# Performance work log

Hardware: AMD Instinct MI355X
Metric: run time of the kernel (lower is better)

The kernel has to match this reference:

```python
import jax, jax.numpy as jnp
import numpy as np

NUM = 8          # group_heads
ALPHA = 1000.0   # Pos_Enc alpha
BETA = 100.0     # Pos_Enc beta


def setup_inputs() -> dict:
    key = jax.random.key(0)
    ks = jax.random.split(key, 19)
    N, C, H = 16384, 64, 1024
    gs1 = H // NUM
    s = 0.02
    r = lambda k, shp: jax.random.normal(k, shp, dtype=jnp.float32) * s
    return {
        "features": jax.random.normal(ks[0], (N, C), dtype=jnp.float32),
        "fc1_w": r(ks[1], (C, H)), "fc1_b": r(ks[2], (H,)),
        "fc2_w": r(ks[3], (H, C)), "fc2_b": r(ks[4], (C,)),
        "g1_w": r(ks[5], (H, H)), "g1_b": r(ks[6], (H,)),
        "g2_w": r(ks[7], (H, H)), "g2_b": r(ks[8], (H,)),
        "gg1_w": r(ks[9], (gs1, gs1)), "gg1_b": r(ks[10], (gs1,)),
        "gg2_w": r(ks[11], (gs1, gs1)), "gg2_b": r(ks[12], (gs1,)),
        "wq": r(ks[13], (H, H)), "wk": r(ks[14], (H, H)), "wv": r(ks[15], (H, H)),
        "wq2": r(ks[16], (gs1, gs1)), "wk2": r(ks[17], (gs1, gs1)),
        "lpe": jax.random.normal(ks[18], (1,), dtype=jnp.float32) * 0.1,
    }


def _mlp(x, w1, b1, w2, b2):
    return jax.nn.relu(x @ w1 + b1) @ w2 + b2


def reference(features, fc1_w, fc1_b, fc2_w, fc2_b, g1_w, g1_b, g2_w, g2_b,
              gg1_w, gg1_b, gg2_w, gg2_b, wq, wk, wv, wq2, wk2, lpe):
    N, C = features.shape
    H = fc1_w.shape[1]
    gs1 = H // NUM   # feature-group size
    gs2 = N // NUM   # token-group size

    x = features @ fc1_w + fc1_b                      # (N, H)

    # --- attn1: per-feature-group vector attention (shared weights -> vectorized)
    xg = x.reshape(N, NUM, gs1)                       # contiguous feature slices
    q1 = xg @ wq2
    k1 = xg @ wk2
    h1 = _mlp(q1 - k1, gg1_w, gg1_b, gg2_w, gg2_b)
    attn1 = jax.nn.softmax(h1 / np.sqrt(gs1).astype(np.float32), axis=0)
    attn1 = attn1.reshape(N, H)                       # concat over groups = reshape

    # --- attn2: source bug: loop uses stale i=NUM-1, so the LAST token group
    # is processed NUM times and tiled along tokens.
    gf2 = x[(NUM - 1) * gs2:, :]                      # (gs2, H)
    q2 = gf2 @ wq
    k2 = gf2 @ wk
    h2 = _mlp(q2 - k2, g1_w, g1_b, g2_w, g2_b)
    a2 = jax.nn.softmax(h2 / np.sqrt(H).astype(np.float32), axis=0)
    attn2 = jnp.tile(a2, (NUM, 1))                    # (N, H)

    attn = attn1 + attn2
    v = x @ wv                                        # (N, H)

    # --- sinusoidal positional encoding (Pos_Enc), only coord-0 slice survives
    xyz = features[:, :3]                             # (N, 3)
    feat_dim = H // 2
    feat_range = jnp.arange(feat_dim, dtype=jnp.float32)
    dim_embed = jnp.power(jnp.float32(ALPHA), feat_range / feat_dim)
    div = BETA * xyz[..., None] / dim_embed           # (N, 3, feat_dim)
    emb = jnp.concatenate([jnp.sin(div), jnp.cos(div)], axis=-1)  # (N, 3, H)
    pe = (emb + lpe[0]) * lpe[0]
    pe0 = pe[:, 0, :]                                 # (N, H) first coordinate

    res = attn * (v + pe0)                            # elementwise einsum bmf,bmf->bmf
    out = res @ fc2_w + fc2_b + features              # residual
    return out
```

## Files before the change

### kernel.cpp

```cpp
#include <hip/hip_runtime.h>
#include <hip/hip_bf16.h>
#include <math.h>
#include <type_traits>


typedef __attribute__((ext_vector_type(8))) short short8;
typedef __attribute__((ext_vector_type(4))) float f32x4;
typedef __attribute__((ext_vector_type(4))) float float4v;

#define GLOAD_LDS16(gptr, lptr)                                                 \
    __builtin_amdgcn_global_load_lds(                                           \
        (const __attribute__((address_space(1))) void*)(gptr),                  \
        (__attribute__((address_space(3))) void*)(lptr), 16, 0, 0)

static __device__ __forceinline__ unsigned short f2bf_bits(float v) {
    __hip_bfloat16 h = __float2bfloat16(v);
    return __builtin_bit_cast(unsigned short, h);
}
static __device__ __forceinline__ float bf_bits2f(unsigned short u) {
    return __bfloat162float(__builtin_bit_cast(__hip_bfloat16, u));
}
static __device__ __forceinline__ int swz16(int r, int c16) {
    return (r << 4) + (c16 ^ (r & 7));
}
static __device__ __forceinline__ int swz_elem(int r, int c) {
    return (r << 7) + ((((c << 1) ^ ((r & 7) << 4))) >> 1);
}
static __device__ __forceinline__ int xcd_swz(int bid, int nwg) {
    return (bid & 7) * (nwg >> 3) + (bid >> 3);
}

static __device__ void conv_t_dev(const float* __restrict__ A, const float* __restrict__ Bsub,
                                  __hip_bfloat16* __restrict__ Ot, int K, int N,
                                  int bx, int by, int tid, float* t )
{
    const int n0 = bx * 32, k0 = by * 32;
    const int tx = tid & 31, ty = tid >> 5;
    #pragma unroll
    for (int j = 0; j < 4; ++j) {
        int k = k0 + ty + j * 8;
        float v = A[(long)k * N + n0 + tx];
        if (Bsub) v -= Bsub[(long)k * N + n0 + tx];
        t[(ty + j * 8) * 33 + tx] = v;
    }
    __syncthreads();
    #pragma unroll
    for (int j = 0; j < 4; ++j) {
        int n = n0 + ty + j * 8;
        Ot[(long)n * K + k0 + tx] = __float2bfloat16(t[tx * 33 + ty + j * 8]);
    }
}

static __device__ void xgemm_dev(const float* __restrict__ features,
                                 const float* __restrict__ fc1_w,
                                 const float* __restrict__ fc1_b,
                                 __hip_bfloat16* __restrict__ xb,
                                 int tile, int tid, char* smem)
{
    unsigned short* As = (unsigned short*)smem;
    unsigned short* Bs = (unsigned short*)(smem + 16384);
    const int bm = (tile >> 3) << 7, bn = (tile & 7) << 7;
    const int wid = tid >> 6, lane = tid & 63;
    const int wm = (wid >> 1) << 6, wn = (wid & 1) << 6;
    const int l15 = lane & 15, kg = lane >> 4;

    #pragma unroll
    for (int i = 0; i < 8; ++i) {
        int idx = i * 256 + tid;
        int r = idx >> 4, c4 = idx & 15;
        float4v f = *(const float4v*)(features + (long)(bm + r) * 64 + c4 * 4);
        unsigned int p0 = f2bf_bits(f[0]) | ((unsigned int)f2bf_bits(f[1]) << 16);
        unsigned int p1 = f2bf_bits(f[2]) | ((unsigned int)f2bf_bits(f[3]) << 16);
        int dst = r * 64 + (((c4 >> 1) ^ (r & 7)) << 3) + (c4 & 1) * 4;
        unsigned int* p = (unsigned int*)&As[dst];
        p[0] = p0; p[1] = p1;
    }
    #pragma unroll
    for (int i = 0; i < 8; ++i) {
        int idx = i * 256 + tid;
        int k = idx >> 5, c4b = idx & 31;
        float4v g = *(const float4v*)(fc1_w + (long)k * 1024 + bn + c4b * 4);
        #pragma unroll
        for (int q = 0; q < 4; ++q) {
            int n = c4b * 4 + q;
            Bs[n * 64 + (((k >> 3) ^ (n & 7)) << 3) + (k & 7)] = f2bf_bits(g[q]);
        }
    }
    __syncthreads();

    f32x4 acc[4][4] = {};
    #pragma unroll
    for (int ks2 = 0; ks2 < 2; ++ks2) {
        const int kslot = ks2 * 4 + kg;
        short8 af[4], bf_[4];
        #pragma unroll
        for (int m = 0; m < 4; ++m) {
            int r = wm + m * 16 + l15;
            af[m] = *(const short8*)&As[r * 64 + ((kslot ^ (r & 7)) << 3)];
        }
        #pragma unroll
        for (int n = 0; n < 4; ++n) {
            int r = wn + n * 16 + l15;
            bf_[n] = *(const short8*)&Bs[r * 64 + ((kslot ^ (r & 7)) << 3)];
        }
        #pragma unroll
        for (int m = 0; m < 4; ++m)
            #pragma unroll
            for (int n = 0; n < 4; ++n)
                acc[m][n] = __builtin_amdgcn_mfma_f32_16x16x32_bf16(
                    af[m], bf_[n], acc[m][n], 0, 0, 0);
    }
    const int rq = kg << 2;
    #pragma unroll
    for (int n = 0; n < 4; ++n) {
        const int col = bn + wn + n * 16 + l15;
        const float bv = fc1_b[col];
        #pragma unroll
        for (int m = 0; m < 4; ++m)
            #pragma unroll
            for (int j = 0; j < 4; ++j)
                xb[(long)(bm + wm + m * 16 + rq + j) * 1024 + col] =
                    __float2bfloat16(acc[m][n][j] + bv);
    }
}

__global__ __launch_bounds__(256) void prep_x_k(
    const float* __restrict__ features, const float* __restrict__ fc1_w,
    const float* __restrict__ fc1_b, const float* __restrict__ fc2_w,
    const float* __restrict__ fc2_b, const float* __restrict__ g1_w,
    const float* __restrict__ g2_w, const float* __restrict__ wq,
    const float* __restrict__ wk, const float* __restrict__ wv,
    const float* __restrict__ wq2, const float* __restrict__ wk2,
    const float* __restrict__ gg1_w, const float* __restrict__ gg2_w,
    __hip_bfloat16* __restrict__ fc2T, __hip_bfloat16* __restrict__ wdT,
    __hip_bfloat16* __restrict__ wvT, __hip_bfloat16* __restrict__ g1T,
    __hip_bfloat16* __restrict__ g2T, __hip_bfloat16* __restrict__ wd2T,
    __hip_bfloat16* __restrict__ gg1T, __hip_bfloat16* __restrict__ gg2T,
    __hip_bfloat16* __restrict__ xb, float* __restrict__ invde,
    float* __restrict__ out)
{
    __shared__ __align__(16) char smem[32768];
    float* t = (float*)smem;
    const int bid = blockIdx.x;
    const int tid = threadIdx.x;

    if (bid == 0) {
        #pragma unroll
        for (int i = 0; i < 2; ++i) {
            int idx = tid + i * 256;
            invde[idx] = exp2f(-9.96578428466209f * (float)idx * (1.f / 512.f));
        }
    } else if (bid < 257) {
        const float4v* f4 = (const float4v*)features;
        float4v* o4 = (float4v*)out;
        const float4v* b4 = (const float4v*)fc2_b;
        long base = (long)(bid - 1) * 1024;
        #pragma unroll
        for (int i = 0; i < 4; ++i) {
            long idx = base + tid + i * 256;
            o4[idx] = f4[idx] + b4[idx & 15];
        }
    } else if (bid < 1281) {
        int tt = bid - 257;  conv_t_dev(wq, wk, wdT, 1024, 1024, tt & 31, tt >> 5, tid, t);
    } else if (bid < 2305) {
        int tt = bid - 1281; conv_t_dev(wv, nullptr, wvT, 1024, 1024, tt & 31, tt >> 5, tid, t);
    } else if (bid < 3329) {
        int tt = bid - 2305; conv_t_dev(g1_w, nullptr, g1T, 1024, 1024, tt & 31, tt >> 5, tid, t);
    } else if (bid < 4353) {
        int tt = bid - 3329; conv_t_dev(g2_w, nullptr, g2T, 1024, 1024, tt & 31, tt >> 5, tid, t);
    } else if (bid < 4417) {
        int tt = bid - 4353; conv_t_dev(fc2_w, nullptr, fc2T, 1024, 64, tt & 1, tt >> 1, tid, t);
    } else if (bid < 4433) {
        int tt = bid - 4417; conv_t_dev(wq2, wk2, wd2T, 128, 128, tt & 3, tt >> 2, tid, t);
    } else if (bid < 4449) {
        int tt = bid - 4433; conv_t_dev(gg1_w, nullptr, gg1T, 128, 128, tt & 3, tt >> 2, tid, t);
    } else if (bid < 4465) {
        int tt = bid - 4449; conv_t_dev(gg2_w, nullptr, gg2T, 128, 128, tt & 3, tt >> 2, tid, t);
    } else {
        xgemm_dev(features, fc1_w, fc1_b, xb, bid - 4465, tid, smem);
    }
}

template <int OP, bool CS>
static __device__ void gemm64_dev(
    const __hip_bfloat16* __restrict__ A, const __hip_bfloat16* __restrict__ Bt,
    const float* __restrict__ bias, __hip_bfloat16* __restrict__ Co,
    float scale, float* __restrict__ pcs, int swz, int tid, char* smem)
{
    const int wid = tid >> 6, lane = tid & 63;
    const int bm = (swz >> 3) << 6, bn = (swz & 7) << 7;
    const int wm = (wid >> 1) << 5, wn = (wid & 1) << 6;
    f32x4 acc[2][4] = {};
    const int rA = tid >> 2, c0 = (tid & 3) << 3;
    const int rB1 = (tid + 256) >> 2;
    const int l15 = lane & 15, kg = lane >> 4;
    const int arow = wm + l15, brow = wn + l15;

#define G64_STAGE(b, k0)                                                        \
    { char* base = smem + (b) * 12288;                                          \
      GLOAD_LDS16(A + (long)(bm + rA) * 1024 + (k0) + c0, base + (wid << 6) * 16); \
      GLOAD_LDS16(Bt + (long)(bn + rA) * 1024 + (k0) + c0,                      \
                  base + 4096 + (wid << 6) * 16);                               \
      GLOAD_LDS16(Bt + (long)(bn + rB1) * 1024 + (k0) + c0,                     \
                  base + 4096 + (256 + (wid << 6)) * 16); }

    G64_STAGE(0, 0);
    #pragma unroll 2
    for (int kt = 0; kt < 32; ++kt) {
        if (kt < 31) {
            G64_STAGE((kt + 1) & 1, (kt + 1) * 32);
            asm volatile("s_waitcnt vmcnt(3)" ::: "memory");
        } else {
            asm volatile("s_waitcnt vmcnt(0)" ::: "memory");
        }
        __builtin_amdgcn_s_barrier();
        __builtin_amdgcn_sched_barrier(0);
        const __hip_bfloat16* As = (const __hip_bfloat16*)(smem + (kt & 1) * 12288);
        const __hip_bfloat16* Bs = (const __hip_bfloat16*)(smem + (kt & 1) * 12288 + 4096);
        short8 af[2], bf_[4];
        #pragma unroll
        for (int m = 0; m < 2; ++m)
            af[m] = ((const short8*)As)[(arow + m * 16) * 4 + kg];
        #pragma unroll
        for (int n = 0; n < 4; ++n)
            bf_[n] = ((const short8*)Bs)[(brow + n * 16) * 4 + kg];
        __builtin_amdgcn_s_setprio(1);
        #pragma unroll
        for (int m = 0; m < 2; ++m)
            #pragma unroll
            for (int n = 0; n < 4; ++n)
                acc[m][n] = __builtin_amdgcn_mfma_f32_16x16x32_bf16(
                    af[m], bf_[n], acc[m][n], 0, 0, 0);
        __builtin_amdgcn_s_setprio(0);
        __builtin_amdgcn_s_barrier();
    }
#undef G64_STAGE

    const int rq = kg << 2;
    float csum[4];
    #pragma unroll
    for (int n = 0; n < 4; ++n) {
        const int col = bn + wn + n * 16 + l15;
        const float bv = bias ? bias[col] : 0.f;
        csum[n] = 0.f;
        #pragma unroll
        for (int m = 0; m < 2; ++m) {
            #pragma unroll
            for (int j = 0; j < 4; ++j) {
                const int row = bm + wm + m * 16 + rq + j;
                float cv = acc[m][n][j] + bv;
                if (OP == 1) cv = fmaxf(cv, 0.f);
                if (OP == 2) cv = __expf(cv * scale);
                if (CS) csum[n] += cv;
                Co[(long)row * 1024 + col] = __float2bfloat16(cv);
            }
        }
    }
    if (CS) {
        __syncthreads();
        float* ps = (float*)smem;
        const int slot = ((wid >> 1) << 2) | kg;
        #pragma unroll
        for (int n = 0; n < 4; ++n)
            ps[(wn + n * 16 + l15) * 8 + slot] = csum[n];
        __syncthreads();
        if (tid < 128) {
            float s = 0.f;
            #pragma unroll
            for (int q = 0; q < 8; ++q) s += ps[tid * 8 + q];
            pcs[(long)(swz >> 3) * 1024 + bn + tid] = s;
        }
    }
}

template <int OP, bool CS>
__global__ __launch_bounds__(256) void gemm64_k(
    const __hip_bfloat16* __restrict__ A, const __hip_bfloat16* __restrict__ Bt,
    const float* __restrict__ bias, __hip_bfloat16* __restrict__ Co,
    float scale, float* __restrict__ pcs)
{
    __shared__ __align__(16) char smem[24576];
    const int swz = xcd_swz(blockIdx.y * gridDim.x + blockIdx.x, gridDim.x * gridDim.y);
    gemm64_dev<OP, CS>(A, Bt, bias, Co, scale, pcs, swz, threadIdx.x, smem);
}

static __device__ void chain_dev(
    const __hip_bfloat16* __restrict__ xb,
    const __hip_bfloat16* __restrict__ w1T,
    const __hip_bfloat16* __restrict__ w2T,
    const __hip_bfloat16* __restrict__ w3T,
    const float* __restrict__ b2, const float* __restrict__ b3,
    __hip_bfloat16* __restrict__ e1, float* __restrict__ pcs1,
    int tileIdx, int tid, char* smem)
{
    unsigned short* act = (unsigned short*)smem;
    unsigned short* Wb  = (unsigned short*)(smem + 32768);
    const int wid = tid >> 6, lane = tid & 63;
    const int wm = (wid >> 1) << 6, wn = (wid & 1) << 6;
    const long tile = (long)tileIdx * (128 * 128);

    #pragma unroll
    for (int i = 0; i < 8; ++i) {
        int L = i * 256 + wid * 64 + lane;
        int r = L >> 4, c16o = (L & 15) ^ (r & 7);
        GLOAD_LDS16(xb + tile + r * 128 + c16o * 8,
                    (char*)act + (i * 256 + wid * 64) * 16);
        GLOAD_LDS16(w1T + r * 128 + c16o * 8,
                    (char*)Wb + (i * 256 + wid * 64) * 16);
    }
    __syncthreads();

    f32x4 acc[4][4];
    const int rq = (lane >> 4) << 2;

#define CHAIN_ZERO()                                                            \
    _Pragma("unroll") for (int m = 0; m < 4; ++m)                               \
        _Pragma("unroll") for (int n = 0; n < 4; ++n)                           \
            acc[m][n] = (f32x4){0.f, 0.f, 0.f, 0.f};

#define CHAIN_MM()                                                              \
    _Pragma("unroll") for (int ks = 0; ks < 4; ++ks) {                          \
        short8 af[4], bfv[4];                                                   \
        const int kc = ks * 4 + (lane >> 4);                                    \
        _Pragma("unroll") for (int m = 0; m < 4; ++m) {                         \
            int r = wm + m * 16 + (lane & 15);                                  \
            af[m] = *(const short8*)((const char*)act + swz16(r, kc) * 16);     \
        }                                                                       \
        _Pragma("unroll") for (int n = 0; n < 4; ++n) {                         \
            int r = wn + n * 16 + (lane & 15);                                  \
            bfv[n] = *(const short8*)((const char*)Wb + swz16(r, kc) * 16);     \
        }                                                                       \
        _Pragma("unroll") for (int m = 0; m < 4; ++m)                           \
            _Pragma("unroll") for (int n = 0; n < 4; ++n)                       \
                acc[m][n] = __builtin_amdgcn_mfma_f32_16x16x32_bf16(            \
                    af[m], bfv[n], acc[m][n], 0, 0, 0);                         \
    }

#define STAGE_W(wptr)                                                           \
    _Pragma("unroll") for (int i = 0; i < 8; ++i) {                             \
        int L = i * 256 + wid * 64 + lane;                                      \
        int r = L >> 4, c16o = (L & 15) ^ (r & 7);                              \
        GLOAD_LDS16((wptr) + r * 128 + c16o * 8,                                \
                    (char*)Wb + (i * 256 + wid * 64) * 16);                     \
    }

    CHAIN_ZERO(); CHAIN_MM();
    __syncthreads();
    STAGE_W(w2T);
    #pragma unroll
    for (int m = 0; m < 4; ++m)
        #pragma unroll
        for (int n = 0; n < 4; ++n)
            #pragma unroll
            for (int j = 0; j < 4; ++j) {
                int row = wm + m * 16 + rq + j, col = wn + n * 16 + (lane & 15);
                act[swz_elem(row, col)] = f2bf_bits(acc[m][n][j]);
            }
    __syncthreads();

    CHAIN_ZERO(); CHAIN_MM();
    __syncthreads();
    STAGE_W(w3T);
    {
        float bv[4];
        #pragma unroll
        for (int n = 0; n < 4; ++n) bv[n] = b2[wn + n * 16 + (lane & 15)];
        #pragma unroll
        for (int m = 0; m < 4; ++m)
            #pragma unroll
            for (int n = 0; n < 4; ++n)
                #pragma unroll
                for (int j = 0; j < 4; ++j) {
                    int row = wm + m * 16 + rq + j, col = wn + n * 16 + (lane & 15);
                    act[swz_elem(row, col)] = f2bf_bits(fmaxf(acc[m][n][j] + bv[n], 0.f));
                }
    }
    __syncthreads();

    CHAIN_ZERO(); CHAIN_MM();
    __syncthreads();
    {
        float bv[4];
        #pragma unroll
        for (int n = 0; n < 4; ++n) bv[n] = b3[wn + n * 16 + (lane & 15)];
        #pragma unroll
        for (int m = 0; m < 4; ++m)
            #pragma unroll
            for (int n = 0; n < 4; ++n)
                #pragma unroll
                for (int j = 0; j < 4; ++j) {
                    int row = wm + m * 16 + rq + j, col = wn + n * 16 + (lane & 15);
                    float ev = __expf((acc[m][n][j] + bv[n]) * 0.08838834764831845f);
                    act[swz_elem(row, col)] = f2bf_bits(ev);
                }
    }
    __syncthreads();

    #pragma unroll
    for (int i = 0; i < 8; ++i) {
        int idx = i * 256 + tid;
        int r = idx >> 4, c16o = idx & 15;
        short8 vd = *(const short8*)((const char*)act + swz16(r, c16o) * 16);
        *(short8*)((__hip_bfloat16*)e1 + tile + r * 128 + c16o * 8) = vd;
    }
    #pragma unroll
    for (int i = 0; i < 4; ++i) {
        int p = i * 256 + tid;
        int g = p >> 7, c = p & 127;
        float s = 0.f;
        #pragma unroll
        for (int t16 = 0; t16 < 16; ++t16) {
            int r = t16 * 8 + g;
            s += bf_bits2f(act[swz_elem(r, c)]);
        }
        pcs1[(long)tileIdx * 1024 + p] = s;
    }
#undef CHAIN_ZERO
#undef CHAIN_MM
#undef STAGE_W
}

__global__ __launch_bounds__(256) void mid_k(
    const __hip_bfloat16* __restrict__ xb, const __hip_bfloat16* __restrict__ wdT,
    __hip_bfloat16* __restrict__ d2b,
    const __hip_bfloat16* __restrict__ wd2T, const __hip_bfloat16* __restrict__ gg1T,
    const __hip_bfloat16* __restrict__ gg2T, const float* __restrict__ gg1_b,
    const float* __restrict__ gg2_b, __hip_bfloat16* __restrict__ e1,
    float* __restrict__ pcs1)
{
    __shared__ __align__(16) char smem[65536];
    const int bid = blockIdx.x, tid = threadIdx.x;
    if (bid < 256) {
        gemm64_dev<0, false>(xb + (size_t)14336 * 1024, wdT, nullptr, d2b,
                             0.f, nullptr, xcd_swz(bid, 256), tid, smem);
    } else {
        chain_dev(xb, wd2T, gg1T, gg2T, gg1_b, gg2_b, e1, pcs1, bid - 256, tid, smem);
    }
}

__global__ __launch_bounds__(1024) void reduce_k(
    const float* __restrict__ pcs1, const float* __restrict__ pcs2,
    float* __restrict__ rcs1, float* __restrict__ rcs2)
{
    __shared__ float red[16][64];
    const int tx = threadIdx.x, ty = threadIdx.y;
    if (blockIdx.x < 16) {
        const int col = blockIdx.x * 64 + tx;
        float s = 0.f;
        for (int p = ty; p < 1024; p += 16) s += pcs1[(long)p * 1024 + col];
        red[ty][tx] = s;
        __syncthreads();
        if (ty == 0) {
            float t = 0.f;
            #pragma unroll
            for (int q = 0; q < 16; ++q) t += red[q][tx];
            rcs1[col] = 1.f / t;
        }
    } else {
        const int col = (blockIdx.x - 16) * 64 + tx;
        float s = 0.f;
        for (int p = ty; p < 32; p += 16) s += pcs2[(long)p * 1024 + col];
        red[ty][tx] = s;
        __syncthreads();
        if (ty == 0) {
            float t = 0.f;
            #pragma unroll
            for (int q = 0; q < 16; ++q) t += red[q][tx];
            rcs2[col] = 1.f / t;
        }
    }
}

__global__ __launch_bounds__(256) void gemm_v_res_out(
    const __hip_bfloat16* __restrict__ A, const __hip_bfloat16* __restrict__ Bt,
    const __hip_bfloat16* __restrict__ e1, const __hip_bfloat16* __restrict__ e2,
    const float* __restrict__ rcs1, const float* __restrict__ rcs2,
    const float* __restrict__ invde, const float* __restrict__ feats,
    const float* __restrict__ lpe, const __hip_bfloat16* __restrict__ fc2T,
    float* __restrict__ out)
{
    __shared__ __align__(16) char smem[65536];
    unsigned short* st = (unsigned short*)smem;

    const int tid = threadIdx.x;
    const int wid = tid >> 6;
    const int lane = tid & 63;
    const int swz = xcd_swz(blockIdx.y * gridDim.x + blockIdx.x, gridDim.x * gridDim.y);
    const int bm = (swz >> 3) << 7, bn = (swz & 7) << 7;
    const int wm = (wid >> 1) << 6, wn = (wid & 1) << 6;

    f32x4 acc[4][4] = {};
    const int c8 = tid & 7;
    const int l15 = lane & 15;
    const int kg = lane >> 4;
    const int arow = wm + l15;
    const int brow = wn + l15;

#define VR_STAGE(b, k0)                                                         \
    { char* base = smem + (b) * 32768;                                          \
      _Pragma("unroll") for (int i = 0; i < 4; ++i) {                           \
        const int r = i * 32 + (tid >> 3);                                      \
        const int c8s = c8 ^ (r & 7);                                           \
        GLOAD_LDS16(A + (long)(bm + r) * 1024 + (k0) + c8s * 8,                 \
                    base + (i * 256 + wid * 64) * 16);                          \
        GLOAD_LDS16(Bt + (long)(bn + r) * 1024 + (k0) + c8s * 8,                \
                    base + 16384 + (i * 256 + wid * 64) * 16); } }

    VR_STAGE(0, 0);
    #pragma unroll 2
    for (int kt = 0; kt < 16; ++kt) {
        if (kt < 15) {
            VR_STAGE((kt + 1) & 1, (kt + 1) * 64);
            asm volatile("s_waitcnt vmcnt(8)" ::: "memory");
        } else {
            asm volatile("s_waitcnt vmcnt(0)" ::: "memory");
        }
        __builtin_amdgcn_s_barrier();
        __builtin_amdgcn_sched_barrier(0);
        const __hip_bfloat16* As = (const __hip_bfloat16*)(smem + (kt & 1) * 32768);
        const __hip_bfloat16* Bs = (const __hip_bfloat16*)(smem + (kt & 1) * 32768 + 16384);
        __builtin_amdgcn_s_setprio(1);
        #pragma unroll
        for (int ks2 = 0; ks2 < 2; ++ks2) {
            const int kslot = ks2 * 4 + kg;
            short8 af[4], bf_[4];
            #pragma unroll
            for (int m = 0; m < 4; ++m) {
                const int r = arow + m * 16;
                af[m] = *(const short8*)(As + (r * 8 + (kslot ^ (r & 7))) * 8);
            }
            #pragma unroll
            for (int n = 0; n < 4; ++n) {
                const int r = brow + n * 16;
                bf_[n] = *(const short8*)(Bs + (r * 8 + (kslot ^ (r & 7))) * 8);
            }
            #pragma unroll
            for (int m = 0; m < 4; ++m)
                #pragma unroll
                for (int n = 0; n < 4; ++n)
                    acc[m][n] = __builtin_amdgcn_mfma_f32_16x16x32_bf16(
                        af[m], bf_[n], acc[m][n], 0, 0, 0);
        }
        __builtin_amdgcn_s_setprio(0);
        __builtin_amdgcn_s_barrier();
    }
#undef VR_STAGE

    const int rq = kg << 2;
    #pragma unroll
    for (int m = 0; m < 4; ++m)
        #pragma unroll
        for (int n = 0; n < 4; ++n)
            #pragma unroll
            for (int j = 0; j < 4; ++j)
                st[(wm + m * 16 + rq + j) * 136 + wn + n * 16 + l15] =
                    f2bf_bits(acc[m][n][j]);
    __syncthreads();

    const float lp = lpe[0];
    #pragma unroll
    for (int p = 0; p < 4; ++p) {
        const int r = p * 32 + (tid >> 3);
        const int cc = (tid & 7) << 4;
        const int grow = bm + r;
        const float angs = 100.f * feats[(long)grow * 64];
        const long goff = (long)grow * 1024 + bn + cc;
        const long goff2 = (long)(grow & 2047) * 1024 + bn + cc;
        short8 ev1[2], ev2[2], sv[2];
        ev1[0] = *(const short8*)((const unsigned short*)e1 + goff);
        ev1[1] = *(const short8*)((const unsigned short*)e1 + goff + 8);
        ev2[0] = *(const short8*)((const unsigned short*)e2 + goff2);
        ev2[1] = *(const short8*)((const unsigned short*)e2 + goff2 + 8);
        sv[0] = *(const short8*)&st[r * 136 + cc];
        sv[1] = *(const short8*)&st[r * 136 + cc + 8];
        unsigned short ov[16];
        #pragma unroll
        for (int q = 0; q < 16; ++q) {
            const int h = bn + cc + q;
            const float ang = angs * invde[h & 511];
            const float tr = (h < 512) ? __sinf(ang) : __cosf(ang);
            const float a = bf_bits2f((unsigned short)ev1[q >> 3][q & 7]) * rcs1[h] +
                            bf_bits2f((unsigned short)ev2[q >> 3][q & 7]) * rcs2[h];
            const float vv = bf_bits2f((unsigned short)sv[q >> 3][q & 7]);
            ov[q] = f2bf_bits(a * (vv + (tr + lp) * lp));
        }
        *(short8*)&st[r * 136 + cc] = *(short8*)&ov[0];
        *(short8*)&st[r * 136 + cc + 8] = *(short8*)&ov[8];
    }
    __syncthreads();

    {
        const int wmO = wid << 5;
        f32x4 aco[2][4] = {};
        #pragma unroll
        for (int ks = 0; ks < 4; ++ks) {
            short8 afo[2], bfo[4];
            #pragma unroll
            for (int m = 0; m < 2; ++m)
                afo[m] = *(const short8*)&st[(wmO + m * 16 + l15) * 136 + ks * 32 + kg * 8];
            #pragma unroll
            for (int n = 0; n < 4; ++n)
                bfo[n] = *(const short8*)((const unsigned short*)fc2T +
                                          (long)(n * 16 + l15) * 1024 + bn + ks * 32 + kg * 8);
            #pragma unroll
            for (int m = 0; m < 2; ++m)
                #pragma unroll
                for (int n = 0; n < 4; ++n)
                    aco[m][n] = __builtin_amdgcn_mfma_f32_16x16x32_bf16(
                        afo[m], bfo[n], aco[m][n], 0, 0, 0);
        }
        #pragma unroll
        for (int m = 0; m < 2; ++m)
            #pragma unroll
            for (int n = 0; n < 4; ++n)
                #pragma unroll
                for (int j = 0; j < 4; ++j) {
                    const int row = bm + wmO + m * 16 + rq + j;
                    atomicAdd(&out[(long)row * 64 + n * 16 + l15], aco[m][n][j]);
                }
    }
}

extern "C" void kernel_launch(void* const* d_in, const int* in_sizes, int n_in,
                              void* d_out, int out_size, void* d_ws, size_t ws_size,
                              hipStream_t stream) {
    const float* features = (const float*)d_in[0];
    const float* fc1_w = (const float*)d_in[1];
    const float* fc1_b = (const float*)d_in[2];
    const float* fc2_w = (const float*)d_in[3];
    const float* fc2_b = (const float*)d_in[4];
    const float* g1_w = (const float*)d_in[5];
    const float* g1_b = (const float*)d_in[6];
    const float* g2_w = (const float*)d_in[7];
    const float* g2_b = (const float*)d_in[8];
    const float* gg1_w = (const float*)d_in[9];
    const float* gg1_b = (const float*)d_in[10];
    const float* gg2_w = (const float*)d_in[11];
    const float* gg2_b = (const float*)d_in[12];
    const float* wq = (const float*)d_in[13];
    const float* wk = (const float*)d_in[14];
    const float* wv = (const float*)d_in[15];
    const float* wq2 = (const float*)d_in[16];
    const float* wk2 = (const float*)d_in[17];
    const float* lpe = (const float*)d_in[18];
    float* out = (float*)d_out;

    char* ws = (char*)d_ws;
    const size_t MB = 1024ull * 1024ull;
    __hip_bfloat16* xb   = (__hip_bfloat16*)ws;
    __hip_bfloat16* e1   = (__hip_bfloat16*)(ws + 32 * MB);
    __hip_bfloat16* d2b  = (__hip_bfloat16*)(ws + 64 * MB);
    __hip_bfloat16* t2b  = (__hip_bfloat16*)(ws + 68 * MB);
    __hip_bfloat16* e2b  = (__hip_bfloat16*)(ws + 72 * MB);
    float*          pcs1 = (float*)(ws + 76 * MB);
    float*          pcs2 = (float*)(ws + 80 * MB);
    char* W = ws + 81 * MB;
    __hip_bfloat16* wdT   = (__hip_bfloat16*)W;
    __hip_bfloat16* wvT   = (__hip_bfloat16*)(W + 2 * MB);
    __hip_bfloat16* g1T   = (__hip_bfloat16*)(W + 4 * MB);
    __hip_bfloat16* g2T   = (__hip_bfloat16*)(W + 6 * MB);
    __hip_bfloat16* fc2T  = (__hip_bfloat16*)(W + 8 * MB);
    __hip_bfloat16* wd2T  = (__hip_bfloat16*)(W + 8 * MB + 256 * 1024);
    __hip_bfloat16* gg1T  = (__hip_bfloat16*)(W + 8 * MB + 320 * 1024);
    __hip_bfloat16* gg2T  = (__hip_bfloat16*)(W + 8 * MB + 384 * 1024);
    float* rcs1  = (float*)(W + 9 * MB);
    float* rcs2  = rcs1 + 1024;
    float* invde = rcs2 + 1024;

    prep_x_k<<<5489, 256, 0, stream>>>(
        features, fc1_w, fc1_b, fc2_w, fc2_b, g1_w, g2_w, wq, wk, wv, wq2, wk2,
        gg1_w, gg2_w, fc2T, wdT, wvT, g1T, g2T, wd2T, gg1T, gg2T, xb, invde, out);

    mid_k<<<1280, 256, 0, stream>>>(xb, wdT, d2b, wd2T, gg1T, gg2T,
                                    gg1_b, gg2_b, e1, pcs1);

    gemm64_k<1, false><<<dim3(8, 32), 256, 0, stream>>>(d2b, g1T, g1_b, t2b, 0.f, nullptr);
    gemm64_k<2, true><<<dim3(8, 32), 256, 0, stream>>>(t2b, g2T, g2_b, e2b, 0.03125f, pcs2);

    reduce_k<<<32, dim3(64, 16), 0, stream>>>(pcs1, pcs2, rcs1, rcs2);

    gemm_v_res_out<<<dim3(8, 128), 256, 0, stream>>>(
        xb, wvT, e1, e2b, rcs1, rcs2, invde, features, lpe, fc2T, out);
}
```

Baseline: 297.8 us.

## Shrink small GEMM tiles to 64x64 and halve K-step in value GEMM

The 2048-row GEMMs (d2, g1, g2) now use 64x64 output tiles instead of 64x128, doubling the block count from 256 to 512 so more of the GPU's CUs are busy. They also gain an XOR swizzle on the LDS layout to avoid bank conflicts. The large v/residual GEMM moves from a 64-wide K step to a 32-wide K step, which halves its LDS footprint (65536 to 34816 bytes) to allow more resident blocks per CU. The cost is that each block reuses less data and the v GEMM runs twice as many loop iterations, each with its own barriers.

```diff
diff --git a/kernel.cpp b/kernel.cpp
--- a/kernel.cpp
+++ b/kernel.cpp
@@ -182,64 +182,66 @@
 }
 
 template <int OP, bool CS>
-static __device__ void gemm64_dev(
+static __device__ void gemm6464_dev(
     const __hip_bfloat16* __restrict__ A, const __hip_bfloat16* __restrict__ Bt,
     const float* __restrict__ bias, __hip_bfloat16* __restrict__ Co,
     float scale, float* __restrict__ pcs, int swz, int tid, char* smem)
 {
     const int wid = tid >> 6, lane = tid & 63;
-    const int bm = (swz >> 3) << 6, bn = (swz & 7) << 7;
-    const int wm = (wid >> 1) << 5, wn = (wid & 1) << 6;
-    f32x4 acc[2][4] = {};
-    const int rA = tid >> 2, c0 = (tid & 3) << 3;
-    const int rB1 = (tid + 256) >> 2;
+    const int bm = (swz >> 4) << 6, bn = (swz & 15) << 6;
+    const int wm = (wid >> 1) << 5, wn = (wid & 1) << 5;
+    f32x4 acc[2][2] = {};
     const int l15 = lane & 15, kg = lane >> 4;
-    const int arow = wm + l15, brow = wn + l15;
-
-#define G64_STAGE(b, k0)                                                        \
-    { char* base = smem + (b) * 12288;                                          \
-      GLOAD_LDS16(A + (long)(bm + rA) * 1024 + (k0) + c0, base + (wid << 6) * 16); \
-      GLOAD_LDS16(Bt + (long)(bn + rA) * 1024 + (k0) + c0,                      \
-                  base + 4096 + (wid << 6) * 16);                               \
-      GLOAD_LDS16(Bt + (long)(bn + rB1) * 1024 + (k0) + c0,                     \
-                  base + 4096 + (256 + (wid << 6)) * 16); }
-
-    G64_STAGE(0, 0);
+    const int rS = tid >> 2;
+    const int c4s = (tid & 3) ^ ((rS >> 1) & 3);
+
+#define G66_STAGE(b, k0)                                                        \
+    { char* base = smem + (b) * 8192;                                           \
+      GLOAD_LDS16(A + (long)(bm + rS) * 1024 + (k0) + c4s * 8,                  \
+                  base + (wid << 6) * 16);                                      \
+      GLOAD_LDS16(Bt + (long)(bn + rS) * 1024 + (k0) + c4s * 8,                 \
+                  base + 4096 + (wid << 6) * 16); }
+
+    G66_STAGE(0, 0);
     #pragma unroll 2
     for (int kt = 0; kt < 32; ++kt) {
         if (kt < 31) {
-            G64_STAGE((kt + 1) & 1, (kt + 1) * 32);
-            asm volatile("s_waitcnt vmcnt(3)" ::: "memory");
+            G66_STAGE((kt + 1) & 1, (kt + 1) * 32);
+            asm volatile("s_waitcnt vmcnt(2)" ::: "memory");
         } else {
             asm volatile("s_waitcnt vmcnt(0)" ::: "memory");
         }
         __builtin_amdgcn_s_barrier();
         __builtin_amdgcn_sched_barrier(0);
-        const __hip_bfloat16* As = (const __hip_bfloat16*)(smem + (kt & 1) * 12288);
-        const __hip_bfloat16* Bs = (const __hip_bfloat16*)(smem + (kt & 1) * 12288 + 4096);
-        short8 af[2], bf_[4];
+        const char* AsB = smem + (kt & 1) * 8192;
+        const char* BsB = AsB + 4096;
+        short8 af[2], bf_[2];
+        #pragma unroll
+        for (int m = 0; m < 2; ++m) {
+            const int R = wm + m * 16 + l15;
+            af[m] = *(const short8*)(AsB + R * 64 + ((kg ^ ((R >> 1) & 3)) << 4));
+        }
+        #pragma unroll
+        for (int n = 0; n < 2; ++n) {
+            const int R = wn + n * 16 + l15;
+            bf_[n] = *(const short8*)(BsB + R * 64 + ((kg ^ ((R >> 1) & 3)) << 4));
+        }
+        __builtin_amdgcn_s_setprio(1);
         #pragma unroll
         for (int m = 0; m < 2; ++m)
-            af[m] = ((const short8*)As)[(arow + m * 16) * 4 + kg];
-        #pragma unroll
-        for (int n = 0; n < 4; ++n)
-            bf_[n] = ((const short8*)Bs)[(brow + n * 16) * 4 + kg];
-        __builtin_amdgcn_s_setprio(1);
-        #pragma unroll
-        for (int m = 0; m < 2; ++m)
-            #pragma unroll
-            for (int n = 0; n < 4; ++n)
+            #pragma unroll
+            for (int n = 0; n < 2; ++n)
                 acc[m][n] = __builtin_amdgcn_mfma_f32_16x16x32_bf16(
                     af[m], bf_[n], acc[m][n], 0, 0, 0);
         __builtin_amdgcn_s_setprio(0);
         __builtin_amdgcn_s_barrier();
     }
-#undef G64_STAGE
+#undef G66_STAGE
 
     const int rq = kg << 2;
-    float csum[4];
-    #pragma unroll
-    for (int n = 0; n < 4; ++n) {
+    float csum[2];
+    #pragma unroll
+    for (int n = 0; n < 2; ++n) {
         const int col = bn + wn + n * 16 + l15;
         const float bv = bias ? bias[col] : 0.f;
         csum[n] = 0.f;
@@ -261,27 +263,27 @@
         float* ps = (float*)smem;
         const int slot = ((wid >> 1) << 2) | kg;
         #pragma unroll
-        for (int n = 0; n < 4; ++n)
+        for (int n = 0; n < 2; ++n)
             ps[(wn + n * 16 + l15) * 8 + slot] = csum[n];
         __syncthreads();
-        if (tid < 128) {
+        if (tid < 64) {
             float s = 0.f;
             #pragma unroll
             for (int q = 0; q < 8; ++q) s += ps[tid * 8 + q];
-            pcs[(long)(swz >> 3) * 1024 + bn + tid] = s;
+            pcs[(long)(swz >> 4) * 1024 + bn + tid] = s;
         }
     }
 }
 
 template <int OP, bool CS>
-__global__ __launch_bounds__(256) void gemm64_k(
+__global__ __launch_bounds__(256) void gemm6464_k(
     const __hip_bfloat16* __restrict__ A, const __hip_bfloat16* __restrict__ Bt,
     const float* __restrict__ bias, __hip_bfloat16* __restrict__ Co,
     float scale, float* __restrict__ pcs)
 {
-    __shared__ __align__(16) char smem[24576];
+    __shared__ __align__(16) char smem[16384];
     const int swz = xcd_swz(blockIdx.y * gridDim.x + blockIdx.x, gridDim.x * gridDim.y);
-    gemm64_dev<OP, CS>(A, Bt, bias, Co, scale, pcs, swz, threadIdx.x, smem);
+    gemm6464_dev<OP, CS>(A, Bt, bias, Co, scale, pcs, swz, threadIdx.x, smem);
 }
 
 static __device__ void chain_dev(
@@ -430,11 +432,11 @@
 {
     __shared__ __align__(16) char smem[65536];
     const int bid = blockIdx.x, tid = threadIdx.x;
-    if (bid < 256) {
-        gemm64_dev<0, false>(xb + (size_t)14336 * 1024, wdT, nullptr, d2b,
-                             0.f, nullptr, xcd_swz(bid, 256), tid, smem);
+    if (bid < 512) {
+        gemm6464_dev<0, false>(xb + (size_t)14336 * 1024, wdT, nullptr, d2b,
+                               0.f, nullptr, xcd_swz(bid, 512), tid, smem);
     } else {
-        chain_dev(xb, wd2T, gg1T, gg2T, gg1_b, gg2_b, e1, pcs1, bid - 256, tid, smem);
+        chain_dev(xb, wd2T, gg1T, gg2T, gg1_b, gg2_b, e1, pcs1, bid - 512, tid, smem);
     }
 }
 
@@ -479,7 +481,7 @@
     const float* __restrict__ lpe, const __hip_bfloat16* __restrict__ fc2T,
     float* __restrict__ out)
 {
-    __shared__ __align__(16) char smem[65536];
+    __shared__ __align__(16) char smem[34816];
     unsigned short* st = (unsigned short*)smem;
 
     const int tid = threadIdx.x;
@@ -490,57 +492,53 @@
     const int wm = (wid >> 1) << 6, wn = (wid & 1) << 6;
 
     f32x4 acc[4][4] = {};
-    const int c8 = tid & 7;
     const int l15 = lane & 15;
     const int kg = lane >> 4;
     const int arow = wm + l15;
     const int brow = wn + l15;
 
 #define VR_STAGE(b, k0)                                                         \
-    { char* base = smem + (b) * 32768;                                          \
-      _Pragma("unroll") for (int i = 0; i < 4; ++i) {                           \
-        const int r = i * 32 + (tid >> 3);                                      \
-        const int c8s = c8 ^ (r & 7);                                           \
-        GLOAD_LDS16(A + (long)(bm + r) * 1024 + (k0) + c8s * 8,                 \
+    { char* base = smem + (b) * 16384;                                          \
+      _Pragma("unroll") for (int i = 0; i < 2; ++i) {                           \
+        const int idx = i * 256 + tid;                                          \
+        const int r = idx >> 2;                                                 \
+        const int c4s = (idx & 3) ^ ((r >> 1) & 3);                             \
+        GLOAD_LDS16(A + (long)(bm + r) * 1024 + (k0) + c4s * 8,                 \
                     base + (i * 256 + wid * 64) * 16);                          \
-        GLOAD_LDS16(Bt + (long)(bn + r) * 1024 + (k0) + c8s * 8,                \
-                    base + 16384 + (i * 256 + wid * 64) * 16); } }
+        GLOAD_LDS16(Bt + (long)(bn + r) * 1024 + (k0) + c4s * 8,                \
+                    base + 8192 + (i * 256 + wid * 64) * 16); } }
 
     VR_STAGE(0, 0);
     #pragma unroll 2
-    for (int kt = 0; kt < 16; ++kt) {
-        if (kt < 15) {
-            VR_STAGE((kt + 1) & 1, (kt + 1) * 64);
-            asm volatile("s_waitcnt vmcnt(8)" ::: "memory");
+    for (int kt = 0; kt < 32; ++kt) {
+        if (kt < 31) {
+            VR_STAGE((kt + 1) & 1, (kt + 1) * 32);
+            asm volatile("s_waitcnt vmcnt(4)" ::: "memory");
         } else {
             asm volatile("s_waitcnt vmcnt(0)" ::: "memory");
         }
         __builtin_amdgcn_s_barrier();
         __builtin_amdgcn_sched_barrier(0);
-        const __hip_bfloat16* As = (const __hip_bfloat16*)(smem + (kt & 1) * 32768);
-        const __hip_bfloat16* Bs = (const __hip_bfloat16*)(smem + (kt & 1) * 32768 + 16384);
+        const char* AsB = smem + (kt & 1) * 16384;
+        const char* BsB = AsB + 8192;
+        short8 af[4], bf_[4];
+        #pragma unroll
+        for (int m = 0; m < 4; ++m) {
+            const int R = arow + m * 16;
+            af[m] = *(const short8*)(AsB + R * 64 + ((kg ^ ((R >> 1) & 3)) << 4));
+        }
+        #pragma unroll
+        for (int n = 0; n < 4; ++n) {
+            const int R = brow + n * 16;
+            bf_[n] = *(const short8*)(BsB + R * 64 + ((kg ^ ((R >> 1) & 3)) << 4));
+        }
         __builtin_amdgcn_s_setprio(1);
         #pragma unroll
-        for (int ks2 = 0; ks2 < 2; ++ks2) {
-            const int kslot = ks2 * 4 + kg;
-            short8 af[4], bf_[4];
-            #pragma unroll
-            for (int m = 0; m < 4; ++m) {
-                const int r = arow + m * 16;
-                af[m] = *(const short8*)(As + (r * 8 + (kslot ^ (r & 7))) * 8);
-            }
-            #pragma unroll
-            for (int n = 0; n < 4; ++n) {
-                const int r = brow + n * 16;
-                bf_[n] = *(const short8*)(Bs + (r * 8 + (kslot ^ (r & 7))) * 8);
-            }
-            #pragma unroll
-            for (int m = 0; m < 4; ++m)
-                #pragma unroll
-                for (int n = 0; n < 4; ++n)
-                    acc[m][n] = __builtin_amdgcn_mfma_f32_16x16x32_bf16(
-                        af[m], bf_[n], acc[m][n], 0, 0, 0);
-        }
+        for (int m = 0; m < 4; ++m)
+            #pragma unroll
+            for (int n = 0; n < 4; ++n)
+                acc[m][n] = __builtin_amdgcn_mfma_f32_16x16x32_bf16(
+                    af[m], bf_[n], acc[m][n], 0, 0, 0);
         __builtin_amdgcn_s_setprio(0);
         __builtin_amdgcn_s_barrier();
     }
@@ -671,11 +669,11 @@
         features, fc1_w, fc1_b, fc2_w, fc2_b, g1_w, g2_w, wq, wk, wv, wq2, wk2,
         gg1_w, gg2_w, fc2T, wdT, wvT, g1T, g2T, wd2T, gg1T, gg2T, xb, invde, out);
 
-    mid_k<<<1280, 256, 0, stream>>>(xb, wdT, d2b, wd2T, gg1T, gg2T,
+    mid_k<<<1536, 256, 0, stream>>>(xb, wdT, d2b, wd2T, gg1T, gg2T,
                                     gg1_b, gg2_b, e1, pcs1);
 
-    gemm64_k<1, false><<<dim3(8, 32), 256, 0, stream>>>(d2b, g1T, g1_b, t2b, 0.f, nullptr);
-    gemm64_k<2, true><<<dim3(8, 32), 256, 0, stream>>>(t2b, g2T, g2_b, e2b, 0.03125f, pcs2);
+    gemm6464_k<1, false><<<dim3(16, 32), 256, 0, stream>>>(d2b, g1T, g1_b, t2b, 0.f, nullptr);
+    gemm6464_k<2, true><<<dim3(16, 32), 256, 0, stream>>>(t2b, g2T, g2_b, e2b, 0.03125f, pcs2);
 
     reduce_k<<<32, dim3(64, 16), 0, stream>>>(pcs1, pcs2, rcs1, rcs2);
 
```

New measurement: 300.7 us. Within noise of the previous version (+1.0%).
